# Optimization experiments

Hardware: AMD Instinct MI355X
Metric: run time of the kernel (lower is better)

## Reference

```python
import jax, jax.numpy as jnp
import numpy as np

N_NODES = 50000
N_EDGES = 800000
IN_DIM = 128
HID_DIM = 128
OUT_DIM = 128
NUM_GRAPHS = 64
NUM_CLASSES = 3


def _glorot(key, shape):
    lim = np.sqrt(6.0 / (shape[0] + shape[1])).astype(np.float32)
    return jax.random.uniform(key, shape, jnp.float32, -lim, lim)


def setup_inputs() -> dict:
    key = jax.random.key(0)
    ks = jax.random.split(key, 10)
    x = jax.random.normal(ks[0], (N_NODES, IN_DIM), jnp.float32)
    edge_index = jax.random.randint(ks[1], (2, N_EDGES), 0, N_NODES, jnp.int32).astype(jnp.int64)
    batch = jnp.sort(jax.random.randint(ks[2], (N_NODES,), 0, NUM_GRAPHS, jnp.int32)).astype(jnp.int64)
    return {
        "x": x,
        "edge_index": edge_index,
        "batch": batch,
        "W1": _glorot(ks[3], (IN_DIM, HID_DIM)),  "b1": jnp.zeros((HID_DIM,), jnp.float32),
        "W2": _glorot(ks[4], (HID_DIM, HID_DIM)), "b2": jnp.zeros((HID_DIM,), jnp.float32),
        "W3": _glorot(ks[5], (HID_DIM, OUT_DIM)), "b3": jnp.zeros((OUT_DIM,), jnp.float32),
        "C1": _glorot(ks[6], (OUT_DIM, HID_DIM)), "bc1": jnp.zeros((HID_DIM,), jnp.float32),
        "C2": _glorot(ks[7], (HID_DIM, NUM_CLASSES)), "bc2": jnp.zeros((NUM_CLASSES,), jnp.float32),
    }


def _gcn_conv(x, src, dst, norm, W, b):
    # PyG GCNConv: linear transform, then normalized gather/scatter aggregation, then bias.
    h = x @ W                               # [N, F_out]
    msg = h[src] * norm[:, None]            # [E+N, F_out] irregular gather
    return jax.ops.segment_sum(msg, dst, num_segments=N_NODES) + b


def reference(x, edge_index, batch, W1, b1, W2, b2, W3, b3, C1, bc1, C2, bc2):
    loops = jnp.arange(N_NODES, dtype=edge_index.dtype)
    src = jnp.concatenate([edge_index[0], loops])  # add self-loops as in GCNConv
    dst = jnp.concatenate([edge_index[1], loops])
    deg = jax.ops.segment_sum(jnp.ones_like(dst, jnp.float32), dst, num_segments=N_NODES)
    dinv = jnp.where(deg > 0, jax.lax.rsqrt(deg), 0.0)
    norm = dinv[src] * dinv[dst]            # symmetric D^-1/2 (A+I) D^-1/2 weights

    # dropout(p=0.2) is identity at inference time
    h = jax.nn.relu(_gcn_conv(x, src, dst, norm, W1, b1))
    h = jax.nn.relu(_gcn_conv(h, src, dst, norm, W2, b2))
    h = _gcn_conv(h, src, dst, norm, W3, b3)

    # global mean pool over batch segment ids
    counts = jax.ops.segment_sum(jnp.ones((N_NODES,), jnp.float32), batch, num_segments=NUM_GRAPHS)
    pooled = jax.ops.segment_sum(h, batch, num_segments=NUM_GRAPHS) / jnp.maximum(counts, 1.0)[:, None]

    g = jax.nn.relu(pooled @ C1 + bc1)      # classifier MLP (dropout 0.3 inactive)
    return g @ C2 + bc2                     # [NUM_GRAPHS, 3]
```

## Files before the change

### kernel.cpp

```cpp
#include <hip/hip_runtime.h>
#include <hip/hip_bf16.h>

#define N_NODES    50000
#define DIM        128
#define NUM_GRAPHS 64
#define NUM_CLASSES 3
#define NPAD       50176
#define XPITCH     136

typedef unsigned short ushort_t;
typedef unsigned int   uint_t;
typedef __attribute__((ext_vector_type(8))) short short8;
typedef __attribute__((ext_vector_type(4))) float f32x4;

__device__ __forceinline__ ushort_t f2bf(float f) {
    union { float f; uint_t u; } v; v.f = f;
    uint_t r = v.u + 0x7fffu + ((v.u >> 16) & 1u);
    return (ushort_t)(r >> 16);
}
__device__ __forceinline__ float bflo(uint_t u) {
    union { uint_t u; float f; } v; v.u = u << 16; return v.f;
}
__device__ __forceinline__ float bfhi(uint_t u) {
    union { uint_t u; float f; } v; v.u = u & 0xffff0000u; return v.f;
}

__device__ __forceinline__ void gather_rl(
    int n, int lane, int myidx0, int p0, int p1,
    const int* __restrict__ csr_src, const uint_t* __restrict__ Tb,
    float2& acc)
{
    uint_t us = Tb[n * 64 + lane];
    float2 a0 = make_float2(bflo(us), bfhi(us));
    float2 a1 = make_float2(0.f, 0.f);
    int deg = p1 - p0;
    if (deg < 0) deg = 0;
    int nchunk = (deg + 63) >> 6;
    int myidx = myidx0;
    for (int ck = 0; ck < nchunk; ++ck) {
        int base = p0 + (ck << 6);
        int cnt = p1 - base; if (cnt > 64) cnt = 64;
        int nb = cnt >> 3;
        if (nb > 0) {
            uint_t ucur[8];
            #pragma unroll
            for (int q = 0; q < 8; ++q)
                ucur[q] = Tb[__builtin_amdgcn_readlane(myidx, q) * 64 + lane];
            for (int b = 1; b < nb; ++b) {
                int jb = b * 8;
                uint_t unxt[8];
                #pragma unroll
                for (int q = 0; q < 8; ++q)
                    unxt[q] = Tb[__builtin_amdgcn_readlane(myidx, jb + q) * 64 + lane];
                #pragma unroll
                for (int q = 0; q < 8; q += 2) {
                    a0.x += bflo(ucur[q]);     a0.y += bfhi(ucur[q]);
                    a1.x += bflo(ucur[q + 1]); a1.y += bfhi(ucur[q + 1]);
                }
                #pragma unroll
                for (int q = 0; q < 8; ++q) ucur[q] = unxt[q];
            }
            #pragma unroll
            for (int q = 0; q < 8; q += 2) {
                a0.x += bflo(ucur[q]);     a0.y += bfhi(ucur[q]);
                a1.x += bflo(ucur[q + 1]); a1.y += bfhi(ucur[q + 1]);
            }
        }
        for (int j = nb * 8; j < cnt; ++j) {
            uint_t u = Tb[__builtin_amdgcn_readlane(myidx, j) * 64 + lane];
            a0.x += bflo(u); a0.y += bfhi(u);
        }
        if (ck + 1 < nchunk) {
            int c2 = p1 - (base + 64);
            myidx = (lane < c2) ? csr_src[base + 64 + lane] : 0;
        }
    }
    acc.x += a0.x + a1.x;
    acc.y += a0.y + a1.y;
}

__global__ void k_init(int* degi, float* pooled, float* counts) {
    int i = blockIdx.x * 256 + threadIdx.x;
    if (i < NPAD) degi[i] = 0;
    if (i < NUM_GRAPHS * DIM) pooled[i] = 0.0f;
    if (i < NUM_GRAPHS) counts[i] = 0.0f;
}

__global__ void k_prep(const float* __restrict__ W1, const float* __restrict__ W2,
                       const float* __restrict__ W3, ushort_t* __restrict__ Wt) {
    int i = blockIdx.x * 256 + threadIdx.x;
    int mat = i >> 14;
    int idx = i & 16383;
    const float* W = (mat == 0) ? W1 : (mat == 1) ? W2 : W3;
    int n = idx >> 7, k = idx & 127;
    Wt[mat * 16384 + n * 128 + k] = f2bf(W[k * 128 + n]);
}

__global__ void k_count(const int* __restrict__ dst, int* degi, int* rank, int nedges) {
    int e = blockIdx.x * 256 + threadIdx.x;
    if (e < nedges) rank[e] = atomicAdd(&degi[dst[e]], 1);
}

__global__ __launch_bounds__(256) void k_scan1(const int* __restrict__ degi,
                                               int* rowptr, int* bsum) {
    __shared__ int sh[256];
    int i = blockIdx.x * 256 + threadIdx.x;
    int v = degi[i];
    sh[threadIdx.x] = v;
    __syncthreads();
    for (int off = 1; off < 256; off <<= 1) {
        int t = (threadIdx.x >= off) ? sh[threadIdx.x - off] : 0;
        __syncthreads();
        sh[threadIdx.x] += t;
        __syncthreads();
    }
    rowptr[i] = sh[threadIdx.x] - v;
    if (threadIdx.x == 255) bsum[blockIdx.x] = sh[255];
}

__global__ __launch_bounds__(256) void k_scan2(int* bsum, int nblocks) {
    __shared__ int sh[256];
    int v = (threadIdx.x < nblocks) ? bsum[threadIdx.x] : 0;
    sh[threadIdx.x] = v;
    __syncthreads();
    for (int off = 1; off < 256; off <<= 1) {
        int t = (threadIdx.x >= off) ? sh[threadIdx.x - off] : 0;
        __syncthreads();
        sh[threadIdx.x] += t;
        __syncthreads();
    }
    if (threadIdx.x < nblocks) bsum[threadIdx.x] = sh[threadIdx.x] - v;
}

__global__ __launch_bounds__(256) void k_scan3(int* rowptr, const int* __restrict__ bsum,
                                               const int* __restrict__ degi,
                                               float* dinv) {
    int i = blockIdx.x * 256 + threadIdx.x;
    rowptr[i] = rowptr[i] + bsum[blockIdx.x];
    if (i < N_NODES) dinv[i] = rsqrtf((float)degi[i] + 1.0f);
}

__global__ void k_fill(const int* __restrict__ src, const int* __restrict__ dst,
                       const int* __restrict__ rank, const int* __restrict__ rowptr,
                       int* csr_src, int nedges) {
    int e = blockIdx.x * 256 + threadIdx.x;
    if (e < nedges) csr_src[rowptr[dst[e]] + rank[e]] = src[e];
}

__global__ __launch_bounds__(256) void k_mm1(
    const float* __restrict__ xin, const ushort_t* __restrict__ WtG,
    const float* __restrict__ dinv, ushort_t* __restrict__ TbOut)
{
    __shared__ ushort_t Wl[DIM * XPITCH];
    __shared__ ushort_t Xl[64 * XPITCH];

    const int tid = threadIdx.x;
    const int rowbase = blockIdx.x * 64;

    #pragma unroll
    for (int i = 0; i < 8; ++i) {
        int g = tid + i * 256;
        uint4 v = ((const uint4*)WtG)[g];
        *((uint4*)&Wl[(g >> 4) * XPITCH + (g & 15) * 8]) = v;
    }
    #pragma unroll
    for (int i = 0; i < 8; ++i) {
        int c = tid + i * 256;
        int row = c >> 5;
        int grow = rowbase + row;
        float4 f = make_float4(0.f, 0.f, 0.f, 0.f);
        if (grow < N_NODES)
            f = ((const float4*)xin)[(long long)rowbase * 32 + c];
        ushort4 h;
        h.x = f2bf(f.x); h.y = f2bf(f.y); h.z = f2bf(f.z); h.w = f2bf(f.w);
        *((ushort4*)&Xl[row * XPITCH + (c & 31) * 4]) = h;
    }
    __syncthreads();

    const int wave = tid >> 6;
    const int lane = tid & 63;
    const int quad = lane >> 4;
    const int lm   = lane & 15;
    const int m0   = wave * 16;

    short8 af[4];
    #pragma unroll
    for (int k0 = 0; k0 < 4; ++k0)
        af[k0] = *(const short8*)&Xl[(m0 + lm) * XPITCH + k0 * 32 + quad * 8];

    int noder[4]; float di[4]; bool okr[4];
    #pragma unroll
    for (int r = 0; r < 4; ++r) {
        noder[r] = rowbase + m0 + quad * 4 + r;
        okr[r] = (noder[r] < N_NODES);
        di[r] = okr[r] ? dinv[noder[r]] : 0.f;
    }

    for (int n0 = 0; n0 < DIM; n0 += 16) {
        f32x4 acc = {0.f, 0.f, 0.f, 0.f};
        #pragma unroll
        for (int k0 = 0; k0 < 4; ++k0) {
            short8 bf = *(const short8*)&Wl[(n0 + lm) * XPITCH + k0 * 32 + quad * 8];
            acc = __builtin_amdgcn_mfma_f32_16x16x32_bf16(af[k0], bf, acc, 0, 0, 0);
        }
        int n = n0 + lm;
        #pragma unroll
        for (int r = 0; r < 4; ++r)
            if (okr[r])
                TbOut[(long long)noder[r] * DIM + n] = f2bf(acc[r] * di[r]);
    }
}

__global__ __launch_bounds__(256) void k_fused(
    const int* __restrict__ rowptr, const int* __restrict__ csr_src,
    const float* __restrict__ dinv, const uint_t* __restrict__ TbIn,
    const ushort_t* __restrict__ WtG, const float* __restrict__ b_prev,
    ushort_t* __restrict__ TbOut)
{
    __shared__ ushort_t Xl[16 * XPITCH];

    const int tid = threadIdx.x;
    const int rowbase = blockIdx.x * 16;
    const int wave = tid >> 6;
    const int lane = tid & 63;

    float2 bias2 = ((const float2*)b_prev)[lane];

    const int nfirst = rowbase + wave * 4;
    int pv = (lane < 5) ? rowptr[nfirst + lane] : 0;
    int p[5];
    #pragma unroll
    for (int i = 0; i < 5; ++i) p[i] = __builtin_amdgcn_readlane(pv, i);

    int idx_n;
    {
        int d0 = p[1] - p[0];
        idx_n = (lane < d0) ? csr_src[p[0] + lane] : 0;
    }

    #pragma unroll
    for (int t = 0; t < 4; ++t) {
        int idx_cur = idx_n;
        if (t < 3) {
            int dn = p[t + 2] - p[t + 1];
            idx_n = (lane < dn) ? csr_src[p[t + 1] + lane] : 0;
        }
        int r = wave * 4 + t;
        int n = rowbase + r;
        float2 acc = make_float2(0.f, 0.f);
        float dd = 0.f;
        if (n < N_NODES) {
            dd = dinv[n];
            gather_rl(n, lane, idx_cur, p[t], p[t + 1], csr_src, TbIn, acc);
        }
        ushort2 h;
        h.x = f2bf(fmaxf(bias2.x + acc.x * dd, 0.f));
        h.y = f2bf(fmaxf(bias2.y + acc.y * dd, 0.f));
        *((ushort2*)&Xl[r * XPITCH + lane * 2]) = h;
    }
    __syncthreads();

    const int quad = lane >> 4;
    const int lm   = lane & 15;

    short8 af[4];
    #pragma unroll
    for (int k0 = 0; k0 < 4; ++k0)
        af[k0] = *(const short8*)&Xl[lm * XPITCH + k0 * 32 + quad * 8];

    int noder[4]; float di[4]; bool okr[4];
    #pragma unroll
    for (int r = 0; r < 4; ++r) {
        noder[r] = rowbase + quad * 4 + r;
        okr[r] = (noder[r] < N_NODES);
        di[r] = okr[r] ? dinv[noder[r]] : 0.f;
    }

    #pragma unroll
    for (int h = 0; h < 2; ++h) {
        int n0 = wave * 32 + h * 16;
        f32x4 acc = {0.f, 0.f, 0.f, 0.f};
        #pragma unroll
        for (int k0 = 0; k0 < 4; ++k0) {
            short8 bf = *(const short8*)&WtG[(n0 + lm) * DIM + k0 * 32 + quad * 8];
            acc = __builtin_amdgcn_mfma_f32_16x16x32_bf16(af[k0], bf, acc, 0, 0, 0);
        }
        int n = n0 + lm;
        #pragma unroll
        for (int r = 0; r < 4; ++r)
            if (okr[r])
                TbOut[(long long)noder[r] * DIM + n] = f2bf(acc[r] * di[r]);
    }
}

__global__ __launch_bounds__(256) void k_poolgather(
    const int* __restrict__ rowptr, const int* __restrict__ csr_src,
    const float* __restrict__ dinv, const uint_t* __restrict__ Tb,
    const float* __restrict__ b3, const int* __restrict__ batch,
    float* pooled, float* counts)
{
    __shared__ float lp[8][DIM];
    __shared__ float lc[8];

    const int tid  = threadIdx.x;
    const int wave = tid >> 6;
    const int lane = tid & 63;
    const int blk0 = blockIdx.x * 32;

    #pragma unroll
    for (int i = 0; i < 4; ++i) ((float*)lp)[tid + i * 256] = 0.f;
    if (tid < 8) lc[tid] = 0.f;
    __syncthreads();

    const int gbase = batch[min(blk0, N_NODES - 1)];
    int n0 = blk0 + wave * 8;

    if (n0 < N_NODES) {
        int nend = min(n0 + 8, N_NODES);
        float2 bias2 = ((const float2*)b3)[lane];

        int pv = (lane < 9) ? rowptr[min(n0 + lane, NPAD)] : 0;
        int p[9];
        #pragma unroll
        for (int i = 0; i < 9; ++i) p[i] = __builtin_amdgcn_readlane(pv, i);

        int cur = batch[n0];
        int runstart = n0;
        float2 pacc = make_float2(0.f, 0.f);

        int idx_n;
        {
            int d0 = p[1] - p[0];
            idx_n = (lane < d0) ? csr_src[p[0] + lane] : 0;
        }

        for (int i = 0; i < nend - n0; ++i) {
            int n = n0 + i;
            int idx_cur = idx_n;
            if (i < 7) {
                int dn = p[i + 2] - p[i + 1];
                idx_n = (lane < dn) ? csr_src[p[i + 1] + lane] : 0;
            }
            int g = batch[n];
            if (g != cur) {
                int slot = cur - gbase;
                if (slot < 8) {
                    atomicAdd(&lp[slot][2 * lane], pacc.x);
                    atomicAdd(&lp[slot][2 * lane + 1], pacc.y);
                    if (lane == 0) atomicAdd(&lc[slot], (float)(n - runstart));
                } else {
                    atomicAdd(&pooled[cur * DIM + 2 * lane], pacc.x);
                    atomicAdd(&pooled[cur * DIM + 2 * lane + 1], pacc.y);
                    if (lane == 0) atomicAdd(&counts[cur], (float)(n - runstart));
                }
                pacc.x = 0.f; pacc.y = 0.f; cur = g; runstart = n;
            }
            float2 acc = make_float2(0.f, 0.f);
            gather_rl(n, lane, idx_cur, p[i], p[i + 1], csr_src, Tb, acc);
            float dd = dinv[n];
            pacc.x += bias2.x + acc.x * dd;
            pacc.y += bias2.y + acc.y * dd;
        }
        int slot = cur - gbase;
        if (slot < 8) {
            atomicAdd(&lp[slot][2 * lane], pacc.x);
            atomicAdd(&lp[slot][2 * lane + 1], pacc.y);
            if (lane == 0) atomicAdd(&lc[slot], (float)(nend - runstart));
        } else {
            atomicAdd(&pooled[cur * DIM + 2 * lane], pacc.x);
            atomicAdd(&pooled[cur * DIM + 2 * lane + 1], pacc.y);
            if (lane == 0) atomicAdd(&counts[cur], (float)(nend - runstart));
        }
    }
    __syncthreads();

    #pragma unroll
    for (int s = 0; s < 8; ++s) {
        if (lc[s] != 0.f) {
            if (tid < DIM) atomicAdd(&pooled[(gbase + s) * DIM + tid], lp[s][tid]);
            if (tid == DIM) atomicAdd(&counts[gbase + s], lc[s]);
        }
    }
}

__global__ __launch_bounds__(128) void k_cls(
    const float* __restrict__ pooled, const float* __restrict__ counts,
    const float* __restrict__ C1, const float* __restrict__ bc1,
    const float* __restrict__ C2, const float* __restrict__ bc2,
    float* out)
{
    __shared__ float pm[DIM];
    __shared__ float gv[DIM];
    int g = blockIdx.x, j = threadIdx.x;
    float cnt = fmaxf(counts[g], 1.0f);
    pm[j] = pooled[g * DIM + j] / cnt;
    __syncthreads();
    float a = bc1[j];
    for (int k = 0; k < DIM; ++k) a += pm[k] * C1[k * DIM + j];
    gv[j] = fmaxf(a, 0.f);
    __syncthreads();
    if (j < NUM_CLASSES) {
        float o = bc2[j];
        for (int k = 0; k < DIM; ++k) o += gv[k] * C2[k * NUM_CLASSES + j];
        out[g * NUM_CLASSES + j] = o;
    }
}

extern "C" void kernel_launch(void* const* d_in, const int* in_sizes, int n_in,
                              void* d_out, int out_size, void* d_ws, size_t ws_size,
                              hipStream_t stream) {
    const float* x    = (const float*)d_in[0];
    const int*   ei   = (const int*)d_in[1];
    const int*   batch= (const int*)d_in[2];
    const float* W1   = (const float*)d_in[3];
    const float* b1   = (const float*)d_in[4];
    const float* W2   = (const float*)d_in[5];
    const float* b2   = (const float*)d_in[6];
    const float* W3   = (const float*)d_in[7];
    const float* b3   = (const float*)d_in[8];
    const float* C1   = (const float*)d_in[9];
    const float* bc1  = (const float*)d_in[10];
    const float* C2   = (const float*)d_in[11];
    const float* bc2  = (const float*)d_in[12];

    const int nedges = in_sizes[1] / 2;
    const int* src = ei;
    const int* dst = ei + nedges;

    float*    dinv    = (float*)d_ws;
    uint_t*   TbA     = (uint_t*)(dinv + NPAD);
    uint_t*   TbB     = TbA + (long long)N_NODES * 64;
    float*    pooled  = (float*)(TbB + (long long)N_NODES * 64);
    float*    counts  = pooled + NUM_GRAPHS * DIM;
    int*      degi    = (int*)(counts + 64);
    int*      rowptr  = degi + NPAD;
    int*      bsum    = rowptr + NPAD + 256;
    int*      rank    = bsum + 256;
    int*      csr_src = rank + nedges;
    ushort_t* Wt      = (ushort_t*)(csr_src + nedges);

    const int nodeBlocks = NPAD / 256;
    const int mmBlocks   = (N_NODES + 63) / 64;
    const int fusedBlocks= (N_NODES + 15) / 16;
    const int pgBlocks   = (N_NODES + 31) / 32;
    const int edgeBlocks = (nedges + 255) / 256;

    k_init<<<nodeBlocks, 256, 0, stream>>>(degi, pooled, counts);
    k_prep<<<192, 256, 0, stream>>>(W1, W2, W3, Wt);
    k_count<<<edgeBlocks, 256, 0, stream>>>(dst, degi, rank, nedges);
    k_scan1<<<nodeBlocks, 256, 0, stream>>>(degi, rowptr, bsum);
    k_scan2<<<1, 256, 0, stream>>>(bsum, nodeBlocks);
    k_scan3<<<nodeBlocks, 256, 0, stream>>>(rowptr, bsum, degi, dinv);
    k_fill<<<edgeBlocks, 256, 0, stream>>>(src, dst, rank, rowptr, csr_src, nedges);

    k_mm1<<<mmBlocks, 256, 0, stream>>>(x, Wt, dinv, (ushort_t*)TbA);
    k_fused<<<fusedBlocks, 256, 0, stream>>>(rowptr, csr_src, dinv, TbA,
                                             Wt + 16384, b1, (ushort_t*)TbB);
    k_fused<<<fusedBlocks, 256, 0, stream>>>(rowptr, csr_src, dinv, TbB,
                                             Wt + 32768, b2, (ushort_t*)TbA);
    k_poolgather<<<pgBlocks, 256, 0, stream>>>(rowptr, csr_src, dinv, TbA,
                                               b3, batch, pooled, counts);
    k_cls<<<NUM_GRAPHS, 128, 0, stream>>>(pooled, counts, C1, bc1, C2, bc2,
                                          (float*)d_out);
}
```

Baseline: 295.0 us.

## Gather two neighbor rows per wave using 8-byte loads per lane

Splits each wave into two half-waves that each fetch a different neighbor's row with 8-byte (uint2) loads. This halves the number of load instructions per edge and doubles the bytes per lane access. The two halves' partial sums are combined with a cross-half shuffle, and output channel indexing is remapped to match. It adds shuffle work, lane-select overhead and an odd-degree tail where one half-wave loads but discards its result.

```diff
diff --git a/kernel.cpp b/kernel.cpp
--- a/kernel.cpp
+++ b/kernel.cpp
@@ -25,14 +25,13 @@
     union { uint_t u; float f; } v; v.u = u & 0xffff0000u; return v.f;
 }
 
-__device__ __forceinline__ void gather_rl(
-    int n, int lane, int myidx0, int p0, int p1,
-    const int* __restrict__ csr_src, const uint_t* __restrict__ Tb,
-    float2& acc)
+__device__ __forceinline__ void pair_gather(
+    int lane, int h, int m, int myidx0, int p0, int p1,
+    const int* __restrict__ csr_src, const uint2* __restrict__ Tb2,
+    float4& A)
 {
-    uint_t us = Tb[n * 64 + lane];
-    float2 a0 = make_float2(bflo(us), bfhi(us));
-    float2 a1 = make_float2(0.f, 0.f);
+    float ax0=0.f, ay0=0.f, az0=0.f, aw0=0.f;
+    float ax1=0.f, ay1=0.f, az1=0.f, aw1=0.f;
     int deg = p1 - p0;
     if (deg < 0) deg = 0;
     int nchunk = (deg + 63) >> 6;
@@ -42,41 +41,68 @@
         int cnt = p1 - base; if (cnt > 64) cnt = 64;
         int nb = cnt >> 3;
         if (nb > 0) {
-            uint_t ucur[8];
+            uint2 ucur[4];
             #pragma unroll
-            for (int q = 0; q < 8; ++q)
-                ucur[q] = Tb[__builtin_amdgcn_readlane(myidx, q) * 64 + lane];
+            for (int q = 0; q < 4; ++q) {
+                int s0 = __builtin_amdgcn_readlane(myidx, 2 * q);
+                int s1 = __builtin_amdgcn_readlane(myidx, 2 * q + 1);
+                int s  = h ? s1 : s0;
+                ucur[q] = Tb2[s * 32 + m];
+            }
             for (int b = 1; b < nb; ++b) {
                 int jb = b * 8;
-                uint_t unxt[8];
+                uint2 unxt[4];
                 #pragma unroll
-                for (int q = 0; q < 8; ++q)
-                    unxt[q] = Tb[__builtin_amdgcn_readlane(myidx, jb + q) * 64 + lane];
-                #pragma unroll
-                for (int q = 0; q < 8; q += 2) {
-                    a0.x += bflo(ucur[q]);     a0.y += bfhi(ucur[q]);
-                    a1.x += bflo(ucur[q + 1]); a1.y += bfhi(ucur[q + 1]);
+                for (int q = 0; q < 4; ++q) {
+                    int s0 = __builtin_amdgcn_readlane(myidx, jb + 2 * q);
+                    int s1 = __builtin_amdgcn_readlane(myidx, jb + 2 * q + 1);
+                    int s  = h ? s1 : s0;
+                    unxt[q] = Tb2[s * 32 + m];
                 }
                 #pragma unroll
-                for (int q = 0; q < 8; ++q) ucur[q] = unxt[q];
+                for (int q = 0; q < 4; q += 2) {
+                    ax0 += bflo(ucur[q].x);     ay0 += bfhi(ucur[q].x);
+                    az0 += bflo(ucur[q].y);     aw0 += bfhi(ucur[q].y);
+                    ax1 += bflo(ucur[q + 1].x); ay1 += bfhi(ucur[q + 1].x);
+                    az1 += bflo(ucur[q + 1].y); aw1 += bfhi(ucur[q + 1].y);
+                }
+                #pragma unroll
+                for (int q = 0; q < 4; ++q) ucur[q] = unxt[q];
             }
             #pragma unroll
-            for (int q = 0; q < 8; q += 2) {
-                a0.x += bflo(ucur[q]);     a0.y += bfhi(ucur[q]);
-                a1.x += bflo(ucur[q + 1]); a1.y += bfhi(ucur[q + 1]);
+            for (int q = 0; q < 4; q += 2) {
+                ax0 += bflo(ucur[q].x);     ay0 += bfhi(ucur[q].x);
+                az0 += bflo(ucur[q].y);     aw0 += bfhi(ucur[q].y);
+                ax1 += bflo(ucur[q + 1].x); ay1 += bfhi(ucur[q + 1].x);
+                az1 += bflo(ucur[q + 1].y); aw1 += bfhi(ucur[q + 1].y);
             }
         }
-        for (int j = nb * 8; j < cnt; ++j) {
-            uint_t u = Tb[__builtin_amdgcn_readlane(myidx, j) * 64 + lane];
-            a0.x += bflo(u); a0.y += bfhi(u);
+        int j = nb * 8;
+        for (; j + 2 <= cnt; j += 2) {
+            int s0 = __builtin_amdgcn_readlane(myidx, j);
+            int s1 = __builtin_amdgcn_readlane(myidx, j + 1);
+            int s  = h ? s1 : s0;
+            uint2 u = Tb2[s * 32 + m];
+            ax0 += bflo(u.x); ay0 += bfhi(u.x);
+            az0 += bflo(u.y); aw0 += bfhi(u.y);
+        }
+        if (j < cnt) {
+            int s = __builtin_amdgcn_readlane(myidx, j);
+            uint2 u = Tb2[s * 32 + m];
+            if (!h) {
+                ax0 += bflo(u.x); ay0 += bfhi(u.x);
+                az0 += bflo(u.y); aw0 += bfhi(u.y);
+            }
         }
         if (ck + 1 < nchunk) {
             int c2 = p1 - (base + 64);
             myidx = (lane < c2) ? csr_src[base + 64 + lane] : 0;
         }
     }
-    acc.x += a0.x + a1.x;
-    acc.y += a0.y + a1.y;
+    A.x += ax0 + ax1;
+    A.y += ay0 + ay1;
+    A.z += az0 + az1;
+    A.w += aw0 + aw1;
 }
 
 __global__ void k_init(int* degi, float* pooled, float* counts) {
@@ -223,8 +249,11 @@
     const int rowbase = blockIdx.x * 16;
     const int wave = tid >> 6;
     const int lane = tid & 63;
-
-    float2 bias2 = ((const float2*)b_prev)[lane];
+    const int h    = lane >> 5;
+    const int m    = lane & 31;
+    const uint2* Tb2 = (const uint2*)TbIn;
+
+    float2 bias2 = ((const float2*)b_prev)[2 * m + h];
 
     const int nfirst = rowbase + wave * 4;
     int pv = (lane < 5) ? rowptr[nfirst + lane] : 0;
@@ -247,16 +276,26 @@
         }
         int r = wave * 4 + t;
         int n = rowbase + r;
-        float2 acc = make_float2(0.f, 0.f);
+        float4 a = make_float4(0.f, 0.f, 0.f, 0.f);
         float dd = 0.f;
+        uint2 us = make_uint2(0u, 0u);
         if (n < N_NODES) {
+            us = Tb2[n * 32 + m];
             dd = dinv[n];
-            gather_rl(n, lane, idx_cur, p[t], p[t + 1], csr_src, TbIn, acc);
-        }
-        ushort2 h;
-        h.x = f2bf(fmaxf(bias2.x + acc.x * dd, 0.f));
-        h.y = f2bf(fmaxf(bias2.y + acc.y * dd, 0.f));
-        *((ushort2*)&Xl[r * XPITCH + lane * 2]) = h;
+            pair_gather(lane, h, m, idx_cur, p[t], p[t + 1], csr_src, Tb2, a);
+        }
+        a.x += __shfl_xor(a.x, 32);
+        a.y += __shfl_xor(a.y, 32);
+        a.z += __shfl_xor(a.z, 32);
+        a.w += __shfl_xor(a.w, 32);
+        a.x += bflo(us.x); a.y += bfhi(us.x);
+        a.z += bflo(us.y); a.w += bfhi(us.y);
+        float o0 = h ? a.z : a.x;
+        float o1 = h ? a.w : a.y;
+        ushort2 hh;
+        hh.x = f2bf(fmaxf(bias2.x + o0 * dd, 0.f));
+        hh.y = f2bf(fmaxf(bias2.y + o1 * dd, 0.f));
+        *((ushort2*)&Xl[r * XPITCH + 4 * m + 2 * h]) = hh;
     }
     __syncthreads();
 
@@ -277,8 +316,8 @@
     }
 
     #pragma unroll
-    for (int h = 0; h < 2; ++h) {
-        int n0 = wave * 32 + h * 16;
+    for (int hh = 0; hh < 2; ++hh) {
+        int n0 = wave * 32 + hh * 16;
         f32x4 acc = {0.f, 0.f, 0.f, 0.f};
         #pragma unroll
         for (int k0 = 0; k0 < 4; ++k0) {
@@ -305,7 +344,11 @@
     const int tid  = threadIdx.x;
     const int wave = tid >> 6;
     const int lane = tid & 63;
+    const int h    = lane >> 5;
+    const int m    = lane & 31;
     const int blk0 = blockIdx.x * 32;
+    const uint2* Tb2 = (const uint2*)Tb;
+    const int ch = 4 * m + 2 * h;
 
     #pragma unroll
     for (int i = 0; i < 4; ++i) ((float*)lp)[tid + i * 256] = 0.f;
@@ -317,7 +360,7 @@
 
     if (n0 < N_NODES) {
         int nend = min(n0 + 8, N_NODES);
-        float2 bias2 = ((const float2*)b3)[lane];
+        float2 bias2 = ((const float2*)b3)[2 * m + h];
 
         int pv = (lane < 9) ? rowptr[min(n0 + lane, NPAD)] : 0;
         int p[9];
@@ -345,30 +388,39 @@
             if (g != cur) {
                 int slot = cur - gbase;
                 if (slot < 8) {
-                    atomicAdd(&lp[slot][2 * lane], pacc.x);
-                    atomicAdd(&lp[slot][2 * lane + 1], pacc.y);
+                    atomicAdd(&lp[slot][ch], pacc.x);
+                    atomicAdd(&lp[slot][ch + 1], pacc.y);
                     if (lane == 0) atomicAdd(&lc[slot], (float)(n - runstart));
                 } else {
-                    atomicAdd(&pooled[cur * DIM + 2 * lane], pacc.x);
-                    atomicAdd(&pooled[cur * DIM + 2 * lane + 1], pacc.y);
+                    atomicAdd(&pooled[cur * DIM + ch], pacc.x);
+                    atomicAdd(&pooled[cur * DIM + ch + 1], pacc.y);
                     if (lane == 0) atomicAdd(&counts[cur], (float)(n - runstart));
                 }
                 pacc.x = 0.f; pacc.y = 0.f; cur = g; runstart = n;
             }
-            float2 acc = make_float2(0.f, 0.f);
-            gather_rl(n, lane, idx_cur, p[i], p[i + 1], csr_src, Tb, acc);
+            float4 a = make_float4(0.f, 0.f, 0.f, 0.f);
+            uint2 us = Tb2[n * 32 + m];
+            pair_gather(lane, h, m, idx_cur, p[i], p[i + 1], csr_src, Tb2, a);
+            a.x += __shfl_xor(a.x, 32);
+            a.y += __shfl_xor(a.y, 32);
+            a.z += __shfl_xor(a.z, 32);
+            a.w += __shfl_xor(a.w, 32);
+            a.x += bflo(us.x); a.y += bfhi(us.x);
+            a.z += bflo(us.y); a.w += bfhi(us.y);
+            float o0 = h ? a.z : a.x;
+            float o1 = h ? a.w : a.y;
             float dd = dinv[n];
-            pacc.x += bias2.x + acc.x * dd;
-            pacc.y += bias2.y + acc.y * dd;
+            pacc.x += bias2.x + o0 * dd;
+            pacc.y += bias2.y + o1 * dd;
         }
         int slot = cur - gbase;
         if (slot < 8) {
-            atomicAdd(&lp[slot][2 * lane], pacc.x);
-            atomicAdd(&lp[slot][2 * lane + 1], pacc.y);
+            atomicAdd(&lp[slot][ch], pacc.x);
+            atomicAdd(&lp[slot][ch + 1], pacc.y);
             if (lane == 0) atomicAdd(&lc[slot], (float)(nend - runstart));
         } else {
-            atomicAdd(&pooled[cur * DIM + 2 * lane], pacc.x);
-            atomicAdd(&pooled[cur * DIM + 2 * lane + 1], pacc.y);
+            atomicAdd(&pooled[cur * DIM + ch], pacc.x);
+            atomicAdd(&pooled[cur * DIM + ch + 1], pacc.y);
             if (lane == 0) atomicAdd(&counts[cur], (float)(nend - runstart));
         }
     }
```

After: 291.0 us. About the same (-1.3%).

## Gather four neighbor rows per wave using 16-byte loads and cross-quad reduction

Applied to the files above, without the earlier changes.

The neighbor gather used to make each wave load one 4-byte bf16 pair per lane from a single neighbor row. It now splits the wave into four 16-lane quads, each fetching a different neighbor row with uint4 loads, and combines the partial sums with xor-shuffles. The aim is fewer, wider memory instructions and about four times fewer serialized row loads per neighbor list. In exchange it adds shuffle reductions, more accumulator registers, and a remapping of channels in the pooling kernel.

```diff
diff --git a/kernel.cpp b/kernel.cpp
--- a/kernel.cpp
+++ b/kernel.cpp
@@ -25,14 +25,24 @@
     union { uint_t u; float f; } v; v.u = u & 0xffff0000u; return v.f;
 }
 
-__device__ __forceinline__ void gather_rl(
-    int n, int lane, int myidx0, int p0, int p1,
-    const int* __restrict__ csr_src, const uint_t* __restrict__ Tb,
-    float2& acc)
+__device__ __forceinline__ void accum8(float* a, uint4 u) {
+    a[0] += bflo(u.x); a[1] += bfhi(u.x);
+    a[2] += bflo(u.y); a[3] += bfhi(u.y);
+    a[4] += bflo(u.z); a[5] += bfhi(u.z);
+    a[6] += bflo(u.w); a[7] += bfhi(u.w);
+}
+
+__device__ __forceinline__ int qsel(int lane, int s0, int s1, int s2, int s3) {
+    int lo = (lane & 16) ? s1 : s0;
+    int hi = (lane & 16) ? s3 : s2;
+    return (lane & 32) ? hi : lo;
+}
+
+__device__ __forceinline__ void quad_gather(
+    int lane, int m, int myidx0, int p0, int p1,
+    const int* __restrict__ csr_src, const uint4* __restrict__ Tb4,
+    float* a)
 {
-    uint_t us = Tb[n * 64 + lane];
-    float2 a0 = make_float2(bflo(us), bfhi(us));
-    float2 a1 = make_float2(0.f, 0.f);
     int deg = p1 - p0;
     if (deg < 0) deg = 0;
     int nchunk = (deg + 63) >> 6;
@@ -42,41 +52,62 @@
         int cnt = p1 - base; if (cnt > 64) cnt = 64;
         int nb = cnt >> 3;
         if (nb > 0) {
-            uint_t ucur[8];
-            #pragma unroll
-            for (int q = 0; q < 8; ++q)
-                ucur[q] = Tb[__builtin_amdgcn_readlane(myidx, q) * 64 + lane];
+            uint4 u0, u1;
+            {
+                int s = qsel(lane, __builtin_amdgcn_readlane(myidx, 0),
+                                   __builtin_amdgcn_readlane(myidx, 1),
+                                   __builtin_amdgcn_readlane(myidx, 2),
+                                   __builtin_amdgcn_readlane(myidx, 3));
+                u0 = Tb4[s * 16 + m];
+                s = qsel(lane, __builtin_amdgcn_readlane(myidx, 4),
+                               __builtin_amdgcn_readlane(myidx, 5),
+                               __builtin_amdgcn_readlane(myidx, 6),
+                               __builtin_amdgcn_readlane(myidx, 7));
+                u1 = Tb4[s * 16 + m];
+            }
             for (int b = 1; b < nb; ++b) {
                 int jb = b * 8;
-                uint_t unxt[8];
-                #pragma unroll
-                for (int q = 0; q < 8; ++q)
-                    unxt[q] = Tb[__builtin_amdgcn_readlane(myidx, jb + q) * 64 + lane];
-                #pragma unroll
-                for (int q = 0; q < 8; q += 2) {
-                    a0.x += bflo(ucur[q]);     a0.y += bfhi(ucur[q]);
-                    a1.x += bflo(ucur[q + 1]); a1.y += bfhi(ucur[q + 1]);
-                }
-                #pragma unroll
-                for (int q = 0; q < 8; ++q) ucur[q] = unxt[q];
+                uint4 n0, n1;
+                int s = qsel(lane, __builtin_amdgcn_readlane(myidx, jb),
+                                   __builtin_amdgcn_readlane(myidx, jb + 1),
+                                   __builtin_amdgcn_readlane(myidx, jb + 2),
+                                   __builtin_amdgcn_readlane(myidx, jb + 3));
+                n0 = Tb4[s * 16 + m];
+                s = qsel(lane, __builtin_amdgcn_readlane(myidx, jb + 4),
+                               __builtin_amdgcn_readlane(myidx, jb + 5),
+                               __builtin_amdgcn_readlane(myidx, jb + 6),
+                               __builtin_amdgcn_readlane(myidx, jb + 7));
+                n1 = Tb4[s * 16 + m];
+                accum8(a, u0); accum8(a, u1);
+                u0 = n0; u1 = n1;
             }
-            #pragma unroll
-            for (int q = 0; q < 8; q += 2) {
-                a0.x += bflo(ucur[q]);     a0.y += bfhi(ucur[q]);
-                a1.x += bflo(ucur[q + 1]); a1.y += bfhi(ucur[q + 1]);
+            accum8(a, u0); accum8(a, u1);
+        }
+        int j = nb * 8;
+        for (; j + 4 <= cnt; j += 4) {
+            int s = qsel(lane, __builtin_amdgcn_readlane(myidx, j),
+                               __builtin_amdgcn_readlane(myidx, j + 1),
+                               __builtin_amdgcn_readlane(myidx, j + 2),
+                               __builtin_amdgcn_readlane(myidx, j + 3));
+            uint4 u = Tb4[s * 16 + m];
+            accum8(a, u);
+        }
+        if (j < cnt) {
+            int rem = cnt - j;
+            int s0 = __builtin_amdgcn_readlane(myidx, j);
+            int s1 = __builtin_amdgcn_readlane(myidx, (j + 1 < cnt) ? j + 1 : j);
+            int s2 = __builtin_amdgcn_readlane(myidx, (j + 2 < cnt) ? j + 2 : j);
+            int s  = qsel(lane, s0, s1, s2, s0);
+            if ((lane >> 4) < rem) {
+                uint4 u = Tb4[s * 16 + m];
+                accum8(a, u);
             }
-        }
-        for (int j = nb * 8; j < cnt; ++j) {
-            uint_t u = Tb[__builtin_amdgcn_readlane(myidx, j) * 64 + lane];
-            a0.x += bflo(u); a0.y += bfhi(u);
         }
         if (ck + 1 < nchunk) {
             int c2 = p1 - (base + 64);
             myidx = (lane < c2) ? csr_src[base + 64 + lane] : 0;
         }
     }
-    acc.x += a0.x + a1.x;
-    acc.y += a0.y + a1.y;
 }
 
 __global__ void k_init(int* degi, float* pooled, float* counts) {
@@ -223,8 +254,11 @@
     const int rowbase = blockIdx.x * 16;
     const int wave = tid >> 6;
     const int lane = tid & 63;
-
-    float2 bias2 = ((const float2*)b_prev)[lane];
+    const int m    = lane & 15;
+    const uint4* Tb4 = (const uint4*)TbIn;
+
+    float4 blo = ((const float4*)b_prev)[m * 2];
+    float4 bhi = ((const float4*)b_prev)[m * 2 + 1];
 
     const int nfirst = rowbase + wave * 4;
     int pv = (lane < 5) ? rowptr[nfirst + lane] : 0;
@@ -247,16 +281,32 @@
         }
         int r = wave * 4 + t;
         int n = rowbase + r;
-        float2 acc = make_float2(0.f, 0.f);
+        float a[8] = {0.f, 0.f, 0.f, 0.f, 0.f, 0.f, 0.f, 0.f};
         float dd = 0.f;
+        uint4 us = make_uint4(0u, 0u, 0u, 0u);
         if (n < N_NODES) {
+            us = Tb4[n * 16 + m];
             dd = dinv[n];
-            gather_rl(n, lane, idx_cur, p[t], p[t + 1], csr_src, TbIn, acc);
-        }
-        ushort2 h;
-        h.x = f2bf(fmaxf(bias2.x + acc.x * dd, 0.f));
-        h.y = f2bf(fmaxf(bias2.y + acc.y * dd, 0.f));
-        *((ushort2*)&Xl[r * XPITCH + lane * 2]) = h;
+            quad_gather(lane, m, idx_cur, p[t], p[t + 1], csr_src, Tb4, a);
+        }
+        #pragma unroll
+        for (int i = 0; i < 8; ++i) {
+            a[i] += __shfl_xor(a[i], 16);
+            a[i] += __shfl_xor(a[i], 32);
+        }
+        accum8(a, us);
+        if (lane < 16) {
+            short8 hh;
+            hh[0] = (short)f2bf(fmaxf(blo.x + a[0] * dd, 0.f));
+            hh[1] = (short)f2bf(fmaxf(blo.y + a[1] * dd, 0.f));
+            hh[2] = (short)f2bf(fmaxf(blo.z + a[2] * dd, 0.f));
+            hh[3] = (short)f2bf(fmaxf(blo.w + a[3] * dd, 0.f));
+            hh[4] = (short)f2bf(fmaxf(bhi.x + a[4] * dd, 0.f));
+            hh[5] = (short)f2bf(fmaxf(bhi.y + a[5] * dd, 0.f));
+            hh[6] = (short)f2bf(fmaxf(bhi.z + a[6] * dd, 0.f));
+            hh[7] = (short)f2bf(fmaxf(bhi.w + a[7] * dd, 0.f));
+            *((short8*)&Xl[r * XPITCH + m * 8]) = hh;
+        }
     }
     __syncthreads();
 
@@ -277,8 +327,8 @@
     }
 
     #pragma unroll
-    for (int h = 0; h < 2; ++h) {
-        int n0 = wave * 32 + h * 16;
+    for (int hh = 0; hh < 2; ++hh) {
+        int n0 = wave * 32 + hh * 16;
         f32x4 acc = {0.f, 0.f, 0.f, 0.f};
         #pragma unroll
         for (int k0 = 0; k0 < 4; ++k0) {
@@ -305,7 +355,11 @@
     const int tid  = threadIdx.x;
     const int wave = tid >> 6;
     const int lane = tid & 63;
+    const int m    = lane & 15;
+    const int q    = lane >> 4;
     const int blk0 = blockIdx.x * 32;
+    const uint4* Tb4 = (const uint4*)Tb;
+    const int ch = 8 * m + 2 * q;
 
     #pragma unroll
     for (int i = 0; i < 4; ++i) ((float*)lp)[tid + i * 256] = 0.f;
@@ -317,7 +371,7 @@
 
     if (n0 < N_NODES) {
         int nend = min(n0 + 8, N_NODES);
-        float2 bias2 = ((const float2*)b3)[lane];
+        float bb0 = b3[ch], bb1 = b3[ch + 1];
 
         int pv = (lane < 9) ? rowptr[min(n0 + lane, NPAD)] : 0;
         int p[9];
@@ -345,30 +399,39 @@
             if (g != cur) {
                 int slot = cur - gbase;
                 if (slot < 8) {
-                    atomicAdd(&lp[slot][2 * lane], pacc.x);
-                    atomicAdd(&lp[slot][2 * lane + 1], pacc.y);
+                    atomicAdd(&lp[slot][ch], pacc.x);
+                    atomicAdd(&lp[slot][ch + 1], pacc.y);
                     if (lane == 0) atomicAdd(&lc[slot], (float)(n - runstart));
                 } else {
-                    atomicAdd(&pooled[cur * DIM + 2 * lane], pacc.x);
-                    atomicAdd(&pooled[cur * DIM + 2 * lane + 1], pacc.y);
+                    atomicAdd(&pooled[cur * DIM + ch], pacc.x);
+                    atomicAdd(&pooled[cur * DIM + ch + 1], pacc.y);
                     if (lane == 0) atomicAdd(&counts[cur], (float)(n - runstart));
                 }
                 pacc.x = 0.f; pacc.y = 0.f; cur = g; runstart = n;
             }
-            float2 acc = make_float2(0.f, 0.f);
-            gather_rl(n, lane, idx_cur, p[i], p[i + 1], csr_src, Tb, acc);
+            float a[8] = {0.f, 0.f, 0.f, 0.f, 0.f, 0.f, 0.f, 0.f};
+            uint4 us = Tb4[n * 16 + m];
+            quad_gather(lane, m, idx_cur, p[i], p[i + 1], csr_src, Tb4, a);
+            #pragma unroll
+            for (int k = 0; k < 8; ++k) {
+                a[k] += __shfl_xor(a[k], 16);
+                a[k] += __shfl_xor(a[k], 32);
+            }
+            accum8(a, us);
+            float x0 = (q == 0) ? a[0] : (q == 1) ? a[2] : (q == 2) ? a[4] : a[6];
+            float x1 = (q == 0) ? a[1] : (q == 1) ? a[3] : (q == 2) ? a[5] : a[7];
             float dd = dinv[n];
-            pacc.x += bias2.x + acc.x * dd;
-            pacc.y += bias2.y + acc.y * dd;
+            pacc.x += bb0 + x0 * dd;
+            pacc.y += bb1 + x1 * dd;
         }
         int slot = cur - gbase;
         if (slot < 8) {
-            atomicAdd(&lp[slot][2 * lane], pacc.x);
-            atomicAdd(&lp[slot][2 * lane + 1], pacc.y);
+            atomicAdd(&lp[slot][ch], pacc.x);
+            atomicAdd(&lp[slot][ch + 1], pacc.y);
             if (lane == 0) atomicAdd(&lc[slot], (float)(nend - runstart));
         } else {
-            atomicAdd(&pooled[cur * DIM + 2 * lane], pacc.x);
-            atomicAdd(&pooled[cur * DIM + 2 * lane + 1], pacc.y);
+            atomicAdd(&pooled[cur * DIM + ch], pacc.x);
+            atomicAdd(&pooled[cur * DIM + ch + 1], pacc.y);
             if (lane == 0) atomicAdd(&counts[cur], (float)(nend - runstart));
         }
     }
```

Result: faster. 285.6 us (-3.2%).
